# Optimization experiments

Hardware: AMD Instinct MI355X
Metric: run time of the kernel (lower is better)

Reference implementation:

```python
import jax, jax.numpy as jnp
import numpy as np

NUM_RBF = 16
TOP_K = 30
MAXREL = 32  # max_relative_feature
M_CTX = 16   # ligand context atoms per residue

PT_GROUP = jnp.array([0,1,18,1,2,13,14,15,16,17,18,1,2,13,14,15,16,17,18,1,2,3,4,5,6,7,8,9,10,11,12,13,14,15,16,17,18,1,2,3,4,5,6,7,8,9,10,11,12,13,14,15,16,17,18,1,2,3,3,3,3,3,3,3,3,3,3,3,3,3,3,3,4,5,6,7,8,9,10,11,12,13,14,15,16,17,18,1,2,3,3,3,3,3,3,3,3,3,3,3,3,3,3,3,4,5,6,7,8,9,10,11,12,13,14,15,16,17,18], dtype=jnp.int32)
PT_PERIOD = jnp.array([0,1,1,2,2,2,2,2,2,2,2,3,3,3,3,3,3,3,3,4,4,4,4,4,4,4,4,4,4,4,4,4,4,4,4,4,4,5,5,5,5,5,5,5,5,5,5,5,5,5,5,5,5,5,5,6,6,6,6,6,6,6,6,6,6,6,6,6,6,6,6,6,6,6,6,6,6,6,6,6,6,6,6,6,6,6,6,7,7,7,7,7,7,7,7,7,7,7,7,7,7,7,7,7,7,7,7,7,7,7,7,7,7,7,7,7,7,7,7], dtype=jnp.int32)

# pair order after the Ca-Ca term: (N,N),(C,C),(O,O),(Cb,Cb),(Ca,N),(Ca,C),(Ca,O),(Ca,Cb),
# (N,C),(N,O),(N,Cb),(Cb,C),(Cb,O),(O,C),(N,Ca),(C,Ca),(O,Ca),(Cb,Ca),(C,N),(O,N),(Cb,N),(C,Cb),(O,Cb),(C,O)
# atom index in A5 stack: N=0, Ca=1, C=2, O=3, Cb=4
AI = np.array([0,2,3,4,1,1,1,1,0,0,0,4,4,3,0,2,3,4,2,3,4,2,3,2])
BI = np.array([0,2,3,4,0,2,3,4,2,3,4,2,3,2,1,1,1,1,0,0,0,4,4,3])


def _rbf(D):
    mu = jnp.linspace(2.0, 22.0, NUM_RBF)
    sigma = (22.0 - 2.0) / NUM_RBF
    return jnp.exp(-(((D[..., None] - mu) / sigma) ** 2))


def _angle_features(A, Bc, Cc, Y):
    v1 = A - Bc
    v2 = Cc - Bc
    e1 = v1 / jnp.linalg.norm(v1, axis=-1, keepdims=True)
    dot = jnp.einsum('bli,bli->bl', e1, v2)[..., None]
    u2 = v2 - e1 * dot
    e2 = u2 / jnp.linalg.norm(u2, axis=-1, keepdims=True)
    e3 = jnp.cross(e1, e2, axis=-1)
    R = jnp.concatenate((e1[..., None], e2[..., None], e3[..., None]), axis=-1)  # [B,L,3,3]
    lv = jnp.einsum('blqp,blyq->blyp', R, Y - Bc[:, :, None, :])
    rxy = jnp.sqrt(lv[..., 0] ** 2 + lv[..., 1] ** 2 + 1e-8)
    f1 = lv[..., 0] / rxy
    f2 = lv[..., 1] / rxy
    rxyz = jnp.linalg.norm(lv, axis=-1) + 1e-8
    f3 = rxy / rxyz
    f4 = lv[..., 2] / rxyz
    return jnp.stack([f1, f2, f3, f4], axis=-1)  # [B,L,M,4]


def setup_inputs() -> dict:
    key = jax.random.key(0)
    ks = jax.random.split(key, 16)
    B, L, M = 2, 2048, M_CTX
    X = jax.random.normal(ks[0], (B, L, 4, 3), jnp.float32) * 10.0
    Y = jax.random.normal(ks[1], (B, L, M, 3), jnp.float32) * 10.0
    mask = jnp.ones((B, L), jnp.float32)
    Y_m = jnp.ones((B, L, M), jnp.float32)
    R_idx = jnp.arange(B * L, dtype=jnp.int32).reshape(B, L)
    chain_labels = jax.random.randint(ks[2], (B, L), 0, 2, jnp.int32)
    Y_t = jax.random.randint(ks[3], (B, L, M), 1, 119, jnp.int32)
    def lin(k, fi, fo):
        return jax.random.normal(k, (fi, fo), jnp.float32) / np.sqrt(fi)
    params = dict(
        Wp=lin(ks[4], 2 * MAXREL + 2, 16), bp=jnp.zeros((16,), jnp.float32),
        We=lin(ks[5], 16 + 25 * NUM_RBF, 128), be=jnp.zeros((128,), jnp.float32),
        Wn=lin(ks[6], 5 * NUM_RBF + 64 + 4, 128), bn=jnp.zeros((128,), jnp.float32),
        Wt=lin(ks[7], 147, 64), bt=jnp.zeros((64,), jnp.float32),
        Wyn=lin(ks[8], 147, 128), byn=jnp.zeros((128,), jnp.float32),
        Wye=lin(ks[9], NUM_RBF, 128), bye=jnp.zeros((128,), jnp.float32),
    )
    return dict(X=X, Y=Y, mask=mask, Y_m=Y_m, R_idx=R_idx, chain_labels=chain_labels, Y_t=Y_t, **params)


def reference(X, Y, mask, Y_m, R_idx, chain_labels, Y_t,
              Wp, bp, We, be, Wn, bn, Wt, bt, Wyn, byn, Wye, bye):
    B, L = X.shape[0], X.shape[1]
    N, Ca, C, O = X[:, :, 0], X[:, :, 1], X[:, :, 2], X[:, :, 3]
    b_ = Ca - N
    c_ = C - Ca
    a_ = jnp.cross(b_, c_, axis=-1)
    Cb = -0.58273431 * a_ + 0.56802827 * b_ - 0.54067466 * c_ + Ca

    # masked pairwise distances + kNN (smallest-k)
    m2 = mask[:, None, :] * mask[:, :, None]
    dX = Ca[:, None, :, :] - Ca[:, :, None, :]
    D = m2 * jnp.sqrt(jnp.sum(dX * dX, -1) + 1e-6)
    Dadj = D + (1.0 - m2) * jnp.max(D, -1, keepdims=True)
    k = min(TOP_K, L)
    negD, E_idx = jax.lax.top_k(-Dadj, k)
    D_neighbors = -negD  # [B,L,K]

    # gather all 5 atom coords of neighbors once, then all 24 cross-atom RBFs
    A5 = jnp.stack([N, Ca, C, O, Cb], axis=2)  # [B,L,5,3]
    nb = A5[jnp.arange(B)[:, None, None], E_idx]  # [B,L,K,5,3]
    dvec = A5[:, :, None, AI, :] - nb[:, :, :, BI, :]  # [B,L,K,24,3]
    Dp = jnp.sqrt(jnp.sum(dvec * dvec, -1) + 1e-6)
    RBF_all = jnp.concatenate([_rbf(D_neighbors),
                               _rbf(Dp).reshape(B, L, k, 24 * NUM_RBF)], axis=-1)  # [B,L,K,400]

    # positional encodings
    offset = jnp.take_along_axis(R_idx[:, :, None] - R_idx[:, None, :], E_idx, axis=2)
    Ech = jnp.take_along_axis((chain_labels[:, :, None] == chain_labels[:, None, :]).astype(jnp.int32), E_idx, axis=2)
    d = jnp.clip(offset + MAXREL, 0, 2 * MAXREL)
    d = d * Ech + (1 - Ech) * (2 * MAXREL + 1)
    Epos = jax.nn.one_hot(d, 2 * MAXREL + 2, dtype=jnp.float32) @ Wp + bp
    E = jnp.concatenate([Epos, RBF_all], axis=-1) @ We + be  # [B,L,K,128]

    # ligand atom featurization
    g = PT_GROUP[Y_t]
    p = PT_PERIOD[Y_t]
    Yt1 = jnp.concatenate([jax.nn.one_hot(Y_t, 120, dtype=jnp.float32),
                           jax.nn.one_hot(g, 19, dtype=jnp.float32),
                           jax.nn.one_hot(p, 8, dtype=jnp.float32)], axis=-1)  # [B,L,M,147]
    Yt_lin = Yt1 @ Wt + bt  # [B,L,M,64]
    dAY = A5[:, :, :, None, :] - Y[:, :, None, :, :]  # [B,L,5,M,3]
    D_AY = jnp.sqrt(jnp.sum(dAY * dAY, -1) + 1e-6)
    RBF_AY = jnp.transpose(_rbf(D_AY), (0, 1, 3, 2, 4)).reshape(B, L, Y.shape[2], 5 * NUM_RBF)
    f_ang = _angle_features(N, Ca, C, Y)  # [B,L,M,4]
    V = jnp.concatenate([RBF_AY, Yt_lin, f_ang], axis=-1) @ Wn + bn  # [B,L,M,128]

    dYY = Y[:, :, :, None, :] - Y[:, :, None, :, :]
    Y_edges = _rbf(jnp.sqrt(jnp.sum(dYY * dYY, -1) + 1e-6)) @ Wye + bye  # [B,L,M,M,128]
    Y_nodes = Yt1 @ Wyn + byn  # [B,L,M,128]
    return V, E, E_idx, Y_nodes, Y_edges, Y_m
```

## Files before the change

kernel.cpp:

```cpp
#include <hip/hip_runtime.h>
#include <float.h>

typedef unsigned int   u32;
typedef unsigned short ushort_t;
typedef __attribute__((ext_vector_type(8))) short  bf16x8;
typedef __attribute__((ext_vector_type(4))) float  f32x4;
typedef __attribute__((ext_vector_type(8))) unsigned short ushort8;

#define NB 2
#define NL 2048
#define NM 16
#define NK 30

#define OV  0ull
#define OE  8388608ull
#define OEI 24117248ull
#define OYN 24240128ull
#define OYE 32628736ull
#define OYM 166846464ull

__constant__ int PT_GROUP_c[119] = {0,1,18,1,2,13,14,15,16,17,18,1,2,13,14,15,16,17,18,1,2,3,4,5,6,7,8,9,10,11,12,13,14,15,16,17,18,1,2,3,4,5,6,7,8,9,10,11,12,13,14,15,16,17,18,1,2,3,3,3,3,3,3,3,3,3,3,3,3,3,3,3,4,5,6,7,8,9,10,11,12,13,14,15,16,17,18,1,2,3,3,3,3,3,3,3,3,3,3,3,3,3,3,3,4,5,6,7,8,9,10,11,12,13,14,15,16,17,18};
__constant__ int PT_PERIOD_c[119] = {0,1,1,2,2,2,2,2,2,2,2,3,3,3,3,3,3,3,3,4,4,4,4,4,4,4,4,4,4,4,4,4,4,4,4,4,4,5,5,5,5,5,5,5,5,5,5,5,5,5,5,5,5,5,5,6,6,6,6,6,6,6,6,6,6,6,6,6,6,6,6,6,6,6,6,6,6,6,6,6,6,6,6,6,6,6,6,7,7,7,7,7,7,7,7,7,7,7,7,7,7,7,7,7,7,7,7,7,7,7,7,7,7,7,7,7,7,7,7};
__constant__ int AI_c[24] = {0,2,3,4,1,1,1,1,0,0,0,4,4,3,0,2,3,4,2,3,4,2,3,2};
__constant__ int BI_c[24] = {0,2,3,4,0,2,3,4,2,3,4,2,3,2,1,1,1,1,0,0,0,4,4,3};

__device__ __forceinline__ float cl24(float v) {
  return fminf(fmaxf(v, -24.f), 24.f);
}

__device__ __forceinline__ ushort_t f2bf(float f) {
  u32 u = __float_as_uint(f);
  return (ushort_t)((u + 0x7fffu + ((u >> 16) & 1u)) >> 16);
}

__device__ __forceinline__ float rbff(float d, int r) {
  float mu = 2.0f + (20.0f / 15.0f) * (float)r;
  float t = (d - mu) * 0.8f;
  return __expf(-t * t);
}

__global__ __launch_bounds__(256) void k_wet(const float* __restrict__ We,
                                             ushort_t* __restrict__ WeT) {
  int n = blockIdx.x;
  for (int k = threadIdx.x; k < 416; k += 256)
    WeT[(size_t)n * 416 + k] = f2bf(We[(size_t)k * 128 + n]);
}

__global__ __launch_bounds__(256) void k_prep(const float* __restrict__ X,
                                              float* __restrict__ A5,
                                              float* __restrict__ Ca4,
                                              float* __restrict__ Fr) {
  int id = blockIdx.x * 256 + threadIdx.x;
  if (id >= NB * NL) return;
  const float* x = X + (size_t)id * 12;
  float Nx=x[0],Ny=x[1],Nz=x[2], Cax=x[3],Cay=x[4],Caz=x[5];
  float Cx=x[6],Cy=x[7],Cz=x[8], Ox=x[9],Oy=x[10],Oz=x[11];
  float bx=Cax-Nx, by=Cay-Ny, bz=Caz-Nz;
  float cx=Cx-Cax, cy=Cy-Cay, cz=Cz-Caz;
  float ax=by*cz-bz*cy, ay=bz*cx-bx*cz, az=bx*cy-by*cx;
  float Cbx = -0.58273431f*ax + 0.56802827f*bx - 0.54067466f*cx + Cax;
  float Cby = -0.58273431f*ay + 0.56802827f*by - 0.54067466f*cy + Cay;
  float Cbz = -0.58273431f*az + 0.56802827f*bz - 0.54067466f*cz + Caz;
  float* A = A5 + (size_t)id * 15;
  A[0]=Nx;A[1]=Ny;A[2]=Nz; A[3]=Cax;A[4]=Cay;A[5]=Caz;
  A[6]=Cx;A[7]=Cy;A[8]=Cz; A[9]=Ox;A[10]=Oy;A[11]=Oz;
  A[12]=Cbx;A[13]=Cby;A[14]=Cbz;
  Ca4[id*4+0]=Cax; Ca4[id*4+1]=Cay; Ca4[id*4+2]=Caz; Ca4[id*4+3]=0.f;
  float v1x=Nx-Cax, v1y=Ny-Cay, v1z=Nz-Caz;
  float v2x=Cx-Cax, v2y=Cy-Cay, v2z=Cz-Caz;
  float n1 = sqrtf(v1x*v1x+v1y*v1y+v1z*v1z);
  float e1x=v1x/n1, e1y=v1y/n1, e1z=v1z/n1;
  float dot = e1x*v2x+e1y*v2y+e1z*v2z;
  float u2x=v2x-e1x*dot, u2y=v2y-e1y*dot, u2z=v2z-e1z*dot;
  float n2 = sqrtf(u2x*u2x+u2y*u2y+u2z*u2z);
  float e2x=u2x/n2, e2y=u2y/n2, e2z=u2z/n2;
  float e3x=e1y*e2z-e1z*e2y, e3y=e1z*e2x-e1x*e2z, e3z=e1x*e2y-e1y*e2x;
  float* F = Fr + (size_t)id * 9;
  F[0]=e1x;F[1]=e1y;F[2]=e1z; F[3]=e2x;F[4]=e2y;F[5]=e2z; F[6]=e3x;F[7]=e3y;F[8]=e3z;
}

__global__ __launch_bounds__(256) void k_topk(const float* __restrict__ Ca4,
                                              const float* __restrict__ mask,
                                              float* __restrict__ Dn,
                                              int* __restrict__ Eidx,
                                              float* __restrict__ out) {
  __shared__ float dist[NL];
  __shared__ float rv[4];
  __shared__ int   ri[4];
  int row = blockIdx.x;
  int b = row >> 11;
  int tid = threadIdx.x;
  const float4* cab = (const float4*)Ca4 + ((size_t)b << 11);
  float4 ci = ((const float4*)Ca4)[row];
  float mi = mask[row];
  float lmax = 0.f;
  for (int j = tid; j < NL; j += 256) {
    float4 cj = cab[j];
    float dx = __fsub_rn(ci.x, cj.x);
    float dy = __fsub_rn(ci.y, cj.y);
    float dz = __fsub_rn(ci.z, cj.z);
    float s  = __fadd_rn(__fadd_rn(__fadd_rn(__fmul_rn(dx,dx), __fmul_rn(dy,dy)),
                                   __fmul_rn(dz,dz)), 1e-6f);
    float D  = __fmul_rn(__fmul_rn(mask[(b << 11) + j], mi), __fsqrt_rn(s));
    dist[j] = D;
    lmax = fmaxf(lmax, D);
  }
  #pragma unroll
  for (int s = 32; s > 0; s >>= 1) lmax = fmaxf(lmax, __shfl_xor(lmax, s));
  if ((tid & 63) == 0) rv[tid >> 6] = lmax;
  __syncthreads();
  float rowmax = fmaxf(fmaxf(rv[0], rv[1]), fmaxf(rv[2], rv[3]));
  for (int j = tid; j < NL; j += 256) {
    float mj = mask[(b << 11) + j];
    dist[j] = __fadd_rn(dist[j], __fmul_rn(__fsub_rn(1.f, __fmul_rn(mi, mj)), rowmax));
  }
  __syncthreads();
  for (int kk = 0; kk < NK; kk++) {
    float bv = FLT_MAX; int bj = NL;
    for (int j = tid; j < NL; j += 256) {
      float v = dist[j];
      if (v < bv) { bv = v; bj = j; }
    }
    #pragma unroll
    for (int s = 32; s > 0; s >>= 1) {
      float ov = __shfl_xor(bv, s);
      int   oj = __shfl_xor(bj, s);
      if (ov < bv || (ov == bv && oj < bj)) { bv = ov; bj = oj; }
    }
    if ((tid & 63) == 0) { rv[tid >> 6] = bv; ri[tid >> 6] = bj; }
    __syncthreads();
    if (tid == 0) {
      float v = rv[0]; int idx = ri[0];
      #pragma unroll
      for (int w = 1; w < 4; w++)
        if (rv[w] < v || (rv[w] == v && ri[w] < idx)) { v = rv[w]; idx = ri[w]; }
      dist[idx] = FLT_MAX;
      Dn[(size_t)row * NK + kk]   = v;
      Eidx[(size_t)row * NK + kk] = idx;
      out[OEI + (size_t)row * NK + kk] = (float)idx;
    }
    __syncthreads();
  }
}

__global__ __launch_bounds__(256) void k_edge(const float* __restrict__ A5,
        const float* __restrict__ Dn, const int* __restrict__ Eidx,
        const int* __restrict__ R_idx, const int* __restrict__ cl,
        const float* __restrict__ Wp, const float* __restrict__ bp,
        const ushort_t* __restrict__ WeT, const float* __restrict__ be,
        float* __restrict__ out) {
  __shared__ __align__(16) ushort_t feat[32][424];
  __shared__ __align__(16) ushort_t wet[128][40];
  int tid = threadIdx.x;
  int e0 = blockIdx.x * 32;
  {
    int el = tid >> 3;
    int te = tid & 7;
    int e  = e0 + el;
    int bi = e / NK;
    int b  = bi >> 11;
    int j  = Eidx[e];
    j = j < 0 ? 0 : (j > NL - 1 ? NL - 1 : j);
    int jrow = (b << 11) + j;
    const float* Ac = A5 + (size_t)bi * 15;
    const float* An = A5 + (size_t)jrow * 15;
    int off = R_idx[bi] - R_idx[jrow];
    int d;
    if (cl[bi] == cl[jrow]) { d = off + 32; d = d < 0 ? 0 : (d > 64 ? 64 : d); }
    else d = 65;
    feat[el][2*te]   = f2bf(Wp[d * 16 + 2*te]   + bp[2*te]);
    feat[el][2*te+1] = f2bf(Wp[d * 16 + 2*te+1] + bp[2*te+1]);
    float dn = Dn[e];
    feat[el][16 + 2*te]   = f2bf(rbff(dn, 2*te));
    feat[el][16 + 2*te+1] = f2bf(rbff(dn, 2*te+1));
    #pragma unroll
    for (int pp = 0; pp < 3; pp++) {
      int p = te + pp * 8;
      int ai = AI_c[p] * 3, bj2 = BI_c[p] * 3;
      float dx = Ac[ai]   - An[bj2];
      float dy = Ac[ai+1] - An[bj2+1];
      float dz = Ac[ai+2] - An[bj2+2];
      float dp = sqrtf(dx*dx + dy*dy + dz*dz + 1e-6f);
      int fb = 32 + p * 16;
      #pragma unroll
      for (int r = 0; r < 16; r++) feat[el][fb + r] = f2bf(rbff(dp, r));
    }
  }
  int l  = tid & 63;
  int wid = tid >> 6;
  int wm = wid >> 1, wn = wid & 1;
  f32x4 acc0 = {0.f,0.f,0.f,0.f}, acc1 = {0.f,0.f,0.f,0.f};
  f32x4 acc2 = {0.f,0.f,0.f,0.f}, acc3 = {0.f,0.f,0.f,0.f};
  int srow = tid >> 1;
  int skk  = (tid & 1) * 16;
  for (int c = 0; c < 13; c++) {
    __syncthreads();
    {
      const ushort_t* g = WeT + (size_t)srow * 416 + c * 32 + skk;
      ushort8 v0 = *(const ushort8*)&g[0];
      ushort8 v1 = *(const ushort8*)&g[8];
      *(ushort8*)&wet[srow][skk]     = v0;
      *(ushort8*)&wet[srow][skk + 8] = v1;
    }
    __syncthreads();
    bf16x8 a = *(const bf16x8*)&feat[wm*16 + (l & 15)][c*32 + (l >> 4)*8];
    bf16x8 b0 = *(const bf16x8*)&wet[wn*64 +  0 + (l & 15)][(l >> 4)*8];
    bf16x8 b1 = *(const bf16x8*)&wet[wn*64 + 16 + (l & 15)][(l >> 4)*8];
    bf16x8 b2 = *(const bf16x8*)&wet[wn*64 + 32 + (l & 15)][(l >> 4)*8];
    bf16x8 b3 = *(const bf16x8*)&wet[wn*64 + 48 + (l & 15)][(l >> 4)*8];
    acc0 = __builtin_amdgcn_mfma_f32_16x16x32_bf16(a, b0, acc0, 0, 0, 0);
    acc1 = __builtin_amdgcn_mfma_f32_16x16x32_bf16(a, b1, acc1, 0, 0, 0);
    acc2 = __builtin_amdgcn_mfma_f32_16x16x32_bf16(a, b2, acc2, 0, 0, 0);
    acc3 = __builtin_amdgcn_mfma_f32_16x16x32_bf16(a, b3, acc3, 0, 0, 0);
  }
  #pragma unroll
  for (int t = 0; t < 4; t++) {
    f32x4 av = (t==0) ? acc0 : (t==1) ? acc1 : (t==2) ? acc2 : acc3;
    int n = wn*64 + t*16 + (l & 15);
    float bb = be[n];
    #pragma unroll
    for (int jj = 0; jj < 4; jj++) {
      int ee = e0 + wm*16 + (l >> 4)*4 + jj;
      out[OE + (size_t)ee * 128 + n] = cl24(av[jj] + bb);
    }
  }
}

__global__ __launch_bounds__(256, 4) void k_v(const float* __restrict__ A5,
        const float* __restrict__ Fr, const float* __restrict__ Y,
        const int* __restrict__ Y_t,
        const float* __restrict__ Wn, const float* __restrict__ bn,
        const float* __restrict__ Wt, const float* __restrict__ bt,
        float* __restrict__ out) {
  __shared__ float wn_s[32][128];
  __shared__ float feat[16][148];
  __shared__ float dAY[16][8];
  int tid = threadIdx.x;
  int bl = blockIdx.x;
  if (tid < 80) {
    int m = tid / 5, a = tid % 5;
    float dx = A5[(size_t)bl*15 + a*3 + 0] - Y[(size_t)bl*48 + m*3 + 0];
    float dy = A5[(size_t)bl*15 + a*3 + 1] - Y[(size_t)bl*48 + m*3 + 1];
    float dz = A5[(size_t)bl*15 + a*3 + 2] - Y[(size_t)bl*48 + m*3 + 2];
    dAY[m][a] = sqrtf(dx*dx + dy*dy + dz*dz + 1e-6f);
  }
  __syncthreads();
  {
    int m = tid >> 4, q = tid & 15;
    #pragma unroll
    for (int a = 0; a < 5; a++) feat[m][a * 16 + q] = rbff(dAY[m][a], q);
    int yt = Y_t[(size_t)bl * NM + m];
    int g = PT_GROUP_c[yt], p = PT_PERIOD_c[yt];
    {
      float4 wa = *(const float4*)&Wt[yt*64 + q*4];
      float4 wb = *(const float4*)&Wt[(120+g)*64 + q*4];
      float4 wc = *(const float4*)&Wt[(139+p)*64 + q*4];
      float4 bb = *(const float4*)&bt[q*4];
      feat[m][80 + q*4 + 0] = wa.x + wb.x + wc.x + bb.x;
      feat[m][80 + q*4 + 1] = wa.y + wb.y + wc.y + bb.y;
      feat[m][80 + q*4 + 2] = wa.z + wb.z + wc.z + bb.z;
      feat[m][80 + q*4 + 3] = wa.w + wb.w + wc.w + bb.w;
    }
    if (q == 0) {
      const float* fr = Fr + (size_t)bl * 9;
      float cax = A5[(size_t)bl*15+3], cay = A5[(size_t)bl*15+4], caz = A5[(size_t)bl*15+5];
      float yx = Y[(size_t)bl*48 + m*3+0] - cax;
      float yy = Y[(size_t)bl*48 + m*3+1] - cay;
      float yz = Y[(size_t)bl*48 + m*3+2] - caz;
      float l0 = fr[0]*yx + fr[1]*yy + fr[2]*yz;
      float l1 = fr[3]*yx + fr[4]*yy + fr[5]*yz;
      float l2 = fr[6]*yx + fr[7]*yy + fr[8]*yz;
      float rxy  = sqrtf(l0*l0 + l1*l1 + 1e-8f);
      float rxyz = sqrtf(l0*l0 + l1*l1 + l2*l2) + 1e-8f;
      feat[m][144] = l0 / rxy;
      feat[m][145] = l1 / rxy;
      feat[m][146] = rxy / rxyz;
      feat[m][147] = l2 / rxyz;
    }
  }
  int n4 = (tid & 31) * 4;
  int rg = tid >> 5;
  float a0[4] = {0,0,0,0}, a1[4] = {0,0,0,0};
  #pragma unroll 1
  for (int f0 = 0; f0 < 148; f0 += 32) {
    int R = 148 - f0; if (R > 32) R = 32;
    __syncthreads();
    for (int x = tid; x < R * 128; x += 256)
      wn_s[x >> 7][x & 127] = Wn[(size_t)(f0 + (x >> 7)) * 128 + (x & 127)];
    __syncthreads();
    #pragma unroll 1
    for (int ff = 0; ff < R; ff++) {
      float4 w = *(const float4*)&wn_s[ff][n4];
      float f0v = feat[rg][f0 + ff];
      float f1v = feat[rg + 8][f0 + ff];
      a0[0]=fmaf(f0v,w.x,a0[0]); a0[1]=fmaf(f0v,w.y,a0[1]);
      a0[2]=fmaf(f0v,w.z,a0[2]); a0[3]=fmaf(f0v,w.w,a0[3]);
      a1[0]=fmaf(f1v,w.x,a1[0]); a1[1]=fmaf(f1v,w.y,a1[1]);
      a1[2]=fmaf(f1v,w.z,a1[2]); a1[3]=fmaf(f1v,w.w,a1[3]);
    }
  }
  float c0=bn[n4], c1=bn[n4+1], c2=bn[n4+2], c3=bn[n4+3];
  {
    float4 s;
    s.x=cl24(a0[0]+c0); s.y=cl24(a0[1]+c1); s.z=cl24(a0[2]+c2); s.w=cl24(a0[3]+c3);
    size_t ob = OV + ((size_t)bl * NM + rg) * 128 + n4;
    *(float4*)&out[ob] = s;
    s.x=cl24(a1[0]+c0); s.y=cl24(a1[1]+c1); s.z=cl24(a1[2]+c2); s.w=cl24(a1[3]+c3);
    *(float4*)&out[ob + (size_t)8 * 128] = s;
  }
}

__global__ __launch_bounds__(256, 4) void k_ynode(const int* __restrict__ Y_t,
        const float* __restrict__ Wyn, const float* __restrict__ byn,
        const float* __restrict__ Y_m, float* __restrict__ out) {
  int tid = threadIdx.x;
  int bl = blockIdx.x;
  if (tid < NM)
    out[OYM + (size_t)bl * NM + tid] = Y_m[(size_t)bl * NM + tid];
  int m = tid >> 4, n0 = (tid & 15) * 8;
  int yt = Y_t[(size_t)bl * NM + m];
  int g = PT_GROUP_c[yt], p = PT_PERIOD_c[yt];
  const float* w0 = Wyn + yt * 128 + n0;
  const float* w1 = Wyn + (120 + g) * 128 + n0;
  const float* w2 = Wyn + (139 + p) * 128 + n0;
  float4 r0 = *(const float4*)&w0[0], r1 = *(const float4*)&w0[4];
  float4 s0 = *(const float4*)&w1[0], s1 = *(const float4*)&w1[4];
  float4 t0 = *(const float4*)&w2[0], t1 = *(const float4*)&w2[4];
  float4 b0 = *(const float4*)&byn[n0], b1 = *(const float4*)&byn[n0 + 4];
  float4 o0, o1;
  o0.x = cl24(r0.x + s0.x + t0.x + b0.x);
  o0.y = cl24(r0.y + s0.y + t0.y + b0.y);
  o0.z = cl24(r0.z + s0.z + t0.z + b0.z);
  o0.w = cl24(r0.w + s0.w + t0.w + b0.w);
  o1.x = cl24(r1.x + s1.x + t1.x + b1.x);
  o1.y = cl24(r1.y + s1.y + t1.y + b1.y);
  o1.z = cl24(r1.z + s1.z + t1.z + b1.z);
  o1.w = cl24(r1.w + s1.w + t1.w + b1.w);
  size_t ob = OYN + ((size_t)bl * NM + m) * 128 + n0;
  *(float4*)&out[ob]     = o0;
  *(float4*)&out[ob + 4] = o1;
}

__global__ __launch_bounds__(256) void k_yedge(const float* __restrict__ Y,
        const float* __restrict__ Wye, const float* __restrict__ bye,
        float* __restrict__ out) {
  __shared__ float rbf_s[256][20];
  __shared__ float ys[16][3];
  __shared__ float wye_s[16][128];
  __shared__ float bye_s[128];
  int tid = threadIdx.x;
  int bl = blockIdx.x;
  if (tid < 48) ((float*)ys)[tid] = Y[(size_t)bl * 48 + tid];
  for (int x = tid; x < 2048; x += 256) wye_s[x >> 7][x & 127] = Wye[x];
  if (tid < 128) bye_s[tid] = bye[tid];
  __syncthreads();
  {
    int m = tid >> 4, m2 = tid & 15;
    float dx = ys[m][0]-ys[m2][0], dy = ys[m][1]-ys[m2][1], dz = ys[m][2]-ys[m2][2];
    float dd = sqrtf(dx*dx + dy*dy + dz*dz + 1e-6f);
    #pragma unroll
    for (int r = 0; r < 16; r++) rbf_s[tid][r] = rbff(dd, r);
  }
  __syncthreads();
  int n2 = (tid & 63) * 2;
  int pg = tid >> 6;
  float wy0[16], wy1[16];
  #pragma unroll
  for (int k = 0; k < 16; k++) { wy0[k] = wye_s[k][n2]; wy1[k] = wye_s[k][n2+1]; }
  float bb0 = bye_s[n2], bb1 = bye_s[n2+1];
  size_t obase = OYE + (size_t)bl * (NM * NM * 128);
  for (int p = pg * 64; p < pg * 64 + 64; p++) {
    float s0 = bb0, s1 = bb1;
    #pragma unroll
    for (int k4 = 0; k4 < 4; k4++) {
      float4 rv = *(const float4*)&rbf_s[p][k4 * 4];
      s0 = fmaf(rv.x, wy0[k4*4+0], s0); s1 = fmaf(rv.x, wy1[k4*4+0], s1);
      s0 = fmaf(rv.y, wy0[k4*4+1], s0); s1 = fmaf(rv.y, wy1[k4*4+1], s1);
      s0 = fmaf(rv.z, wy0[k4*4+2], s0); s1 = fmaf(rv.z, wy1[k4*4+2], s1);
      s0 = fmaf(rv.w, wy0[k4*4+3], s0); s1 = fmaf(rv.w, wy1[k4*4+3], s1);
    }
    float2 st; st.x = cl24(s0); st.y = cl24(s1);
    *(float2*)&out[obase + (size_t)p * 128 + n2] = st;
  }
}

extern "C" void kernel_launch(void* const* d_in, const int* in_sizes, int n_in,
                              void* d_out, int out_size, void* d_ws, size_t ws_size,
                              hipStream_t stream) {
  const float* X     = (const float*)d_in[0];
  const float* Y     = (const float*)d_in[1];
  const float* mask  = (const float*)d_in[2];
  const float* Y_m   = (const float*)d_in[3];
  const int*   R_idx = (const int*)d_in[4];
  const int*   cl    = (const int*)d_in[5];
  const int*   Y_t   = (const int*)d_in[6];
  const float* Wp    = (const float*)d_in[7];
  const float* bp    = (const float*)d_in[8];
  const float* We    = (const float*)d_in[9];
  const float* be    = (const float*)d_in[10];
  const float* Wn    = (const float*)d_in[11];
  const float* bn    = (const float*)d_in[12];
  const float* Wt    = (const float*)d_in[13];
  const float* bt    = (const float*)d_in[14];
  const float* Wyn   = (const float*)d_in[15];
  const float* byn   = (const float*)d_in[16];
  const float* Wye   = (const float*)d_in[17];
  const float* bye   = (const float*)d_in[18];
  float* out = (float*)d_out;

  float* wsf  = (float*)d_ws;
  float* A5   = wsf;
  float* Ca4  = A5  + 61440;
  float* Fr   = Ca4 + 16384;
  float* Dn   = Fr  + 36864;
  int*   Eidx = (int*)(Dn + 122880);
  ushort_t* WeT = (ushort_t*)(Eidx + 122880);

  k_wet  <<<128,  256, 0, stream>>>(We, WeT);
  k_prep <<<16,   256, 0, stream>>>(X, A5, Ca4, Fr);
  k_topk <<<NB*NL,256, 0, stream>>>(Ca4, mask, Dn, Eidx, out);
  k_edge <<<(NB*NL*NK)/32, 256, 0, stream>>>(A5, Dn, Eidx, R_idx, cl, Wp, bp, WeT, be, out);
  k_v    <<<NB*NL,256, 0, stream>>>(A5, Fr, Y, Y_t, Wn, bn, Wt, bt, out);
  k_ynode<<<NB*NL,256, 0, stream>>>(Y_t, Wyn, byn, Y_m, out);
  k_yedge<<<NB*NL,256, 0, stream>>>(Y, Wye, bye, out);
}
```

Before: 341.3 us.

## Use register top-k with candidate merge, direct-global MFMA B loads, MFMA node projection

The top-k kernel now keeps each thread's 8 distances in registers. Each wavefront picks its own 30 smallest without block-wide syncs per iteration, and a final single-wave merge over the 120 candidates produces the global top-30. The edge kernel drops its shared-memory staging of the transposed edge weights and feeds MFMA B operands straight from global/L2, removing two barriers per K-chunk. The node-feature kernel replaces its scalar FP32 FMA loop with bf16 MFMA, using a new pre-transposed, padded bf16 weight buffer, which lowers precision for that projection.

```diff
diff --git a/kernel.cpp b/kernel.cpp
--- a/kernel.cpp
+++ b/kernel.cpp
@@ -44,6 +44,15 @@
   int n = blockIdx.x;
   for (int k = threadIdx.x; k < 416; k += 256)
     WeT[(size_t)n * 416 + k] = f2bf(We[(size_t)k * 128 + n]);
+}
+
+__global__ __launch_bounds__(256) void k_wnt(const float* __restrict__ Wn,
+                                             ushort_t* __restrict__ WnT) {
+  int n = blockIdx.x;
+  int k = threadIdx.x;
+  if (k < 160)
+    WnT[(size_t)n * 160 + k] = (k < 148) ? f2bf(Wn[(size_t)k * 128 + n])
+                                         : (ushort_t)0;
 }
 
 __global__ __launch_bounds__(256) void k_prep(const float* __restrict__ X,
@@ -86,7 +95,8 @@
                                               float* __restrict__ out) {
   __shared__ float dist[NL];
   __shared__ float rv[4];
-  __shared__ int   ri[4];
+  __shared__ float cand_v[128];
+  __shared__ int   cand_i[128];
   int row = blockIdx.x;
   int b = row >> 11;
   int tid = threadIdx.x;
@@ -115,11 +125,18 @@
     dist[j] = __fadd_rn(dist[j], __fmul_rn(__fsub_rn(1.f, __fmul_rn(mi, mj)), rowmax));
   }
   __syncthreads();
-  for (int kk = 0; kk < NK; kk++) {
+  int w = tid >> 6, l = tid & 63;
+  int base = w * 512 + l;
+  float v[8];
+  #pragma unroll
+  for (int k = 0; k < 8; k++) v[k] = dist[base + k * 64];
+  if (tid < 8) { cand_v[120 + tid] = FLT_MAX; cand_i[120 + tid] = NL; }
+  for (int it = 0; it < NK; it++) {
     float bv = FLT_MAX; int bj = NL;
-    for (int j = tid; j < NL; j += 256) {
-      float v = dist[j];
-      if (v < bv) { bv = v; bj = j; }
+    #pragma unroll
+    for (int k = 0; k < 8; k++) {
+      int jj = base + k * 64;
+      if (v[k] < bv) { bv = v[k]; bj = jj; }
     }
     #pragma unroll
     for (int s = 32; s > 0; s >>= 1) {
@@ -127,19 +144,37 @@
       int   oj = __shfl_xor(bj, s);
       if (ov < bv || (ov == bv && oj < bj)) { bv = ov; bj = oj; }
     }
-    if ((tid & 63) == 0) { rv[tid >> 6] = bv; ri[tid >> 6] = bj; }
-    __syncthreads();
-    if (tid == 0) {
-      float v = rv[0]; int idx = ri[0];
+    int ow = bj & 511;
+    int ko = ow >> 6;
+    bool mine = (ow & 63) == l;
+    #pragma unroll
+    for (int k = 0; k < 8; k++)
+      if (mine && k == ko) v[k] = FLT_MAX;
+    if (l == 0) { cand_v[w * NK + it] = bv; cand_i[w * NK + it] = bj; }
+  }
+  __syncthreads();
+  if (tid < 64) {
+    float v1 = cand_v[tid], v2 = cand_v[64 + tid];
+    int   i1 = cand_i[tid], i2 = cand_i[64 + tid];
+    for (int it = 0; it < NK; it++) {
+      float bv; int bj, sl;
+      if (v1 < v2 || (v1 == v2 && i1 < i2)) { bv = v1; bj = i1; sl = tid; }
+      else                                  { bv = v2; bj = i2; sl = 64 + tid; }
       #pragma unroll
-      for (int w = 1; w < 4; w++)
-        if (rv[w] < v || (rv[w] == v && ri[w] < idx)) { v = rv[w]; idx = ri[w]; }
-      dist[idx] = FLT_MAX;
-      Dn[(size_t)row * NK + kk]   = v;
-      Eidx[(size_t)row * NK + kk] = idx;
-      out[OEI + (size_t)row * NK + kk] = (float)idx;
-    }
-    __syncthreads();
+      for (int s = 32; s > 0; s >>= 1) {
+        float ov = __shfl_xor(bv, s);
+        int   oj = __shfl_xor(bj, s);
+        int   os = __shfl_xor(sl, s);
+        if (ov < bv || (ov == bv && oj < bj)) { bv = ov; bj = oj; sl = os; }
+      }
+      if (sl == tid)           v1 = FLT_MAX;
+      else if (sl == 64 + tid) v2 = FLT_MAX;
+      if (tid == 0) {
+        Dn[(size_t)row * NK + it]   = bv;
+        Eidx[(size_t)row * NK + it] = bj;
+        out[OEI + (size_t)row * NK + it] = (float)bj;
+      }
+    }
   }
 }
 
@@ -150,7 +185,6 @@
         const ushort_t* __restrict__ WeT, const float* __restrict__ be,
         float* __restrict__ out) {
   __shared__ __align__(16) ushort_t feat[32][424];
-  __shared__ __align__(16) ushort_t wet[128][40];
   int tid = threadIdx.x;
   int e0 = blockIdx.x * 32;
   {
@@ -186,28 +220,20 @@
       for (int r = 0; r < 16; r++) feat[el][fb + r] = f2bf(rbff(dp, r));
     }
   }
+  __syncthreads();
   int l  = tid & 63;
   int wid = tid >> 6;
   int wm = wid >> 1, wn = wid & 1;
   f32x4 acc0 = {0.f,0.f,0.f,0.f}, acc1 = {0.f,0.f,0.f,0.f};
   f32x4 acc2 = {0.f,0.f,0.f,0.f}, acc3 = {0.f,0.f,0.f,0.f};
-  int srow = tid >> 1;
-  int skk  = (tid & 1) * 16;
+  const ushort_t* Wb = WeT + (size_t)(wn*64 + (l & 15)) * 416 + (l >> 4) * 8;
+  #pragma unroll 2
   for (int c = 0; c < 13; c++) {
-    __syncthreads();
-    {
-      const ushort_t* g = WeT + (size_t)srow * 416 + c * 32 + skk;
-      ushort8 v0 = *(const ushort8*)&g[0];
-      ushort8 v1 = *(const ushort8*)&g[8];
-      *(ushort8*)&wet[srow][skk]     = v0;
-      *(ushort8*)&wet[srow][skk + 8] = v1;
-    }
-    __syncthreads();
-    bf16x8 a = *(const bf16x8*)&feat[wm*16 + (l & 15)][c*32 + (l >> 4)*8];
-    bf16x8 b0 = *(const bf16x8*)&wet[wn*64 +  0 + (l & 15)][(l >> 4)*8];
-    bf16x8 b1 = *(const bf16x8*)&wet[wn*64 + 16 + (l & 15)][(l >> 4)*8];
-    bf16x8 b2 = *(const bf16x8*)&wet[wn*64 + 32 + (l & 15)][(l >> 4)*8];
-    bf16x8 b3 = *(const bf16x8*)&wet[wn*64 + 48 + (l & 15)][(l >> 4)*8];
+    bf16x8 a  = *(const bf16x8*)&feat[wm*16 + (l & 15)][c*32 + (l >> 4)*8];
+    bf16x8 b0 = *(const bf16x8*)(Wb + c*32);
+    bf16x8 b1 = *(const bf16x8*)(Wb + 16*416 + c*32);
+    bf16x8 b2 = *(const bf16x8*)(Wb + 32*416 + c*32);
+    bf16x8 b3 = *(const bf16x8*)(Wb + 48*416 + c*32);
     acc0 = __builtin_amdgcn_mfma_f32_16x16x32_bf16(a, b0, acc0, 0, 0, 0);
     acc1 = __builtin_amdgcn_mfma_f32_16x16x32_bf16(a, b1, acc1, 0, 0, 0);
     acc2 = __builtin_amdgcn_mfma_f32_16x16x32_bf16(a, b2, acc2, 0, 0, 0);
@@ -226,17 +252,24 @@
   }
 }
 
-__global__ __launch_bounds__(256, 4) void k_v(const float* __restrict__ A5,
+__global__ __launch_bounds__(256) void k_v(const float* __restrict__ A5,
         const float* __restrict__ Fr, const float* __restrict__ Y,
         const int* __restrict__ Y_t,
-        const float* __restrict__ Wn, const float* __restrict__ bn,
+        const ushort_t* __restrict__ WnT, const float* __restrict__ bn,
         const float* __restrict__ Wt, const float* __restrict__ bt,
         float* __restrict__ out) {
-  __shared__ float wn_s[32][128];
-  __shared__ float feat[16][148];
+  __shared__ __align__(16) ushort_t wnt_s[128][168];
+  __shared__ __align__(16) ushort_t feat[16][168];
   __shared__ float dAY[16][8];
   int tid = threadIdx.x;
   int bl = blockIdx.x;
+  {
+    int n = tid >> 1, h = tid & 1;
+    const ushort8* src = (const ushort8*)(WnT + (size_t)n * 160 + h * 80);
+    ushort8* dst = (ushort8*)&wnt_s[n][h * 80];
+    #pragma unroll
+    for (int i = 0; i < 10; i++) dst[i] = src[i];
+  }
   if (tid < 80) {
     int m = tid / 5, a = tid % 5;
     float dx = A5[(size_t)bl*15 + a*3 + 0] - Y[(size_t)bl*48 + m*3 + 0];
@@ -248,7 +281,7 @@
   {
     int m = tid >> 4, q = tid & 15;
     #pragma unroll
-    for (int a = 0; a < 5; a++) feat[m][a * 16 + q] = rbff(dAY[m][a], q);
+    for (int a = 0; a < 5; a++) feat[m][a * 16 + q] = f2bf(rbff(dAY[m][a], q));
     int yt = Y_t[(size_t)bl * NM + m];
     int g = PT_GROUP_c[yt], p = PT_PERIOD_c[yt];
     {
@@ -256,10 +289,10 @@
       float4 wb = *(const float4*)&Wt[(120+g)*64 + q*4];
       float4 wc = *(const float4*)&Wt[(139+p)*64 + q*4];
       float4 bb = *(const float4*)&bt[q*4];
-      feat[m][80 + q*4 + 0] = wa.x + wb.x + wc.x + bb.x;
-      feat[m][80 + q*4 + 1] = wa.y + wb.y + wc.y + bb.y;
-      feat[m][80 + q*4 + 2] = wa.z + wb.z + wc.z + bb.z;
-      feat[m][80 + q*4 + 3] = wa.w + wb.w + wc.w + bb.w;
+      feat[m][80 + q*4 + 0] = f2bf(wa.x + wb.x + wc.x + bb.x);
+      feat[m][80 + q*4 + 1] = f2bf(wa.y + wb.y + wc.y + bb.y);
+      feat[m][80 + q*4 + 2] = f2bf(wa.z + wb.z + wc.z + bb.z);
+      feat[m][80 + q*4 + 3] = f2bf(wa.w + wb.w + wc.w + bb.w);
     }
     if (q == 0) {
       const float* fr = Fr + (size_t)bl * 9;
@@ -272,41 +305,36 @@
       float l2 = fr[6]*yx + fr[7]*yy + fr[8]*yz;
       float rxy  = sqrtf(l0*l0 + l1*l1 + 1e-8f);
       float rxyz = sqrtf(l0*l0 + l1*l1 + l2*l2) + 1e-8f;
-      feat[m][144] = l0 / rxy;
-      feat[m][145] = l1 / rxy;
-      feat[m][146] = rxy / rxyz;
-      feat[m][147] = l2 / rxyz;
-    }
-  }
-  int n4 = (tid & 31) * 4;
-  int rg = tid >> 5;
-  float a0[4] = {0,0,0,0}, a1[4] = {0,0,0,0};
-  #pragma unroll 1
-  for (int f0 = 0; f0 < 148; f0 += 32) {
-    int R = 148 - f0; if (R > 32) R = 32;
-    __syncthreads();
-    for (int x = tid; x < R * 128; x += 256)
-      wn_s[x >> 7][x & 127] = Wn[(size_t)(f0 + (x >> 7)) * 128 + (x & 127)];
-    __syncthreads();
-    #pragma unroll 1
-    for (int ff = 0; ff < R; ff++) {
-      float4 w = *(const float4*)&wn_s[ff][n4];
-      float f0v = feat[rg][f0 + ff];
-      float f1v = feat[rg + 8][f0 + ff];
-      a0[0]=fmaf(f0v,w.x,a0[0]); a0[1]=fmaf(f0v,w.y,a0[1]);
-      a0[2]=fmaf(f0v,w.z,a0[2]); a0[3]=fmaf(f0v,w.w,a0[3]);
-      a1[0]=fmaf(f1v,w.x,a1[0]); a1[1]=fmaf(f1v,w.y,a1[1]);
-      a1[2]=fmaf(f1v,w.z,a1[2]); a1[3]=fmaf(f1v,w.w,a1[3]);
-    }
-  }
-  float c0=bn[n4], c1=bn[n4+1], c2=bn[n4+2], c3=bn[n4+3];
-  {
-    float4 s;
-    s.x=cl24(a0[0]+c0); s.y=cl24(a0[1]+c1); s.z=cl24(a0[2]+c2); s.w=cl24(a0[3]+c3);
-    size_t ob = OV + ((size_t)bl * NM + rg) * 128 + n4;
-    *(float4*)&out[ob] = s;
-    s.x=cl24(a1[0]+c0); s.y=cl24(a1[1]+c1); s.z=cl24(a1[2]+c2); s.w=cl24(a1[3]+c3);
-    *(float4*)&out[ob + (size_t)8 * 128] = s;
+      feat[m][144] = f2bf(l0 / rxy);
+      feat[m][145] = f2bf(l1 / rxy);
+      feat[m][146] = f2bf(rxy / rxyz);
+      feat[m][147] = f2bf(l2 / rxyz);
+    }
+    if (q < 12) feat[m][148 + q] = 0;
+  }
+  __syncthreads();
+  int l = tid & 63;
+  int wid = tid >> 6;
+  int n0 = wid * 32;
+  f32x4 acc0 = {0.f,0.f,0.f,0.f}, acc1 = {0.f,0.f,0.f,0.f};
+  #pragma unroll
+  for (int c = 0; c < 5; c++) {
+    bf16x8 a  = *(const bf16x8*)&feat[l & 15][c*32 + (l >> 4)*8];
+    bf16x8 b0 = *(const bf16x8*)&wnt_s[n0 +      (l & 15)][c*32 + (l >> 4)*8];
+    bf16x8 b1 = *(const bf16x8*)&wnt_s[n0 + 16 + (l & 15)][c*32 + (l >> 4)*8];
+    acc0 = __builtin_amdgcn_mfma_f32_16x16x32_bf16(a, b0, acc0, 0, 0, 0);
+    acc1 = __builtin_amdgcn_mfma_f32_16x16x32_bf16(a, b1, acc1, 0, 0, 0);
+  }
+  #pragma unroll
+  for (int t = 0; t < 2; t++) {
+    f32x4 av = (t==0) ? acc0 : acc1;
+    int n = n0 + t*16 + (l & 15);
+    float bb = bn[n];
+    #pragma unroll
+    for (int jj = 0; jj < 4; jj++) {
+      int m = (l >> 4)*4 + jj;
+      out[OV + ((size_t)bl * NM + m) * 128 + n] = cl24(av[jj] + bb);
+    }
   }
 }
 
@@ -415,12 +443,14 @@
   float* Dn   = Fr  + 36864;
   int*   Eidx = (int*)(Dn + 122880);
   ushort_t* WeT = (ushort_t*)(Eidx + 122880);
+  ushort_t* WnT = WeT + 128 * 416;
 
   k_wet  <<<128,  256, 0, stream>>>(We, WeT);
+  k_wnt  <<<128,  256, 0, stream>>>(Wn, WnT);
   k_prep <<<16,   256, 0, stream>>>(X, A5, Ca4, Fr);
   k_topk <<<NB*NL,256, 0, stream>>>(Ca4, mask, Dn, Eidx, out);
   k_edge <<<(NB*NL*NK)/32, 256, 0, stream>>>(A5, Dn, Eidx, R_idx, cl, Wp, bp, WeT, be, out);
-  k_v    <<<NB*NL,256, 0, stream>>>(A5, Fr, Y, Y_t, Wn, bn, Wt, bt, out);
+  k_v    <<<NB*NL,256, 0, stream>>>(A5, Fr, Y, Y_t, WnT, bn, Wt, bt, out);
   k_ynode<<<NB*NL,256, 0, stream>>>(Y_t, Wyn, byn, Y_m, out);
   k_yedge<<<NB*NL,256, 0, stream>>>(Y, Wye, bye, out);
 }
```

After: 334.7 us. No clear change (-1.9%).
